# Kernel optimization log

Measured on AMD Instinct MI355X. Metric: run time of the kernel, lower is better.

The kernel has to match this reference:

```python
import jax, jax.numpy as jnp
import numpy as np

H, W, HID = 7, 7, 512
IN_DIM = 1024

def _grid_edges(h, w):
    e = []
    for r in range(h):
        for c in range(w):
            n = r * w + c
            if c < w - 1:
                e.append((n, n + 1))
            if r < h - 1:
                e.append((n, n + w))
    return np.asarray(e, dtype=np.int32).T  # [2, 84]

_BASE = _grid_edges(H, W)

def setup_inputs() -> dict:
    key = jax.random.key(0)
    ks = jax.random.split(key, 16)
    B = 1024
    s = 0.02
    return {
        "visual_feat": jax.random.normal(ks[0], (B, 512, H, W), jnp.float32),
        "tactile_feat": jax.random.normal(ks[1], (B, 512, H, W), jnp.float32),
        "proj_W": jax.random.normal(ks[2], (IN_DIM, 2), jnp.float32) * s,
        "proj_b": jnp.zeros((2,), jnp.float32),
        "gc1_rel_W": jax.random.normal(ks[3], (IN_DIM, HID), jnp.float32) * s,
        "gc1_rel_b": jnp.zeros((HID,), jnp.float32),
        "gc1_root_W": jax.random.normal(ks[4], (IN_DIM, HID), jnp.float32) * s,
        "bn1_gamma": jnp.ones((HID,), jnp.float32),
        "bn1_beta": jnp.zeros((HID,), jnp.float32),
        "gc2_rel_W": jax.random.normal(ks[5], (HID, HID), jnp.float32) * s,
        "gc2_rel_b": jnp.zeros((HID,), jnp.float32),
        "gc2_root_W": jax.random.normal(ks[6], (HID, HID), jnp.float32) * s,
        "bn2_gamma": jnp.ones((HID,), jnp.float32),
        "bn2_beta": jnp.zeros((HID,), jnp.float32),
        "dec_W": jax.random.normal(ks[7], (HID + 1, HID), jnp.float32) * s,
        "dec_b": jnp.zeros((HID,), jnp.float32),
    }

def _batched_edges(B):
    off = (np.arange(B, dtype=np.int32) * (H * W))[:, None]
    src = (_BASE[0][None, :] + off).reshape(-1)
    dst = (_BASE[1][None, :] + off).reshape(-1)
    return jnp.asarray(src), jnp.asarray(dst)

def _bn(x, gamma, beta):
    mu = x.mean(0)
    var = x.var(0)  # biased, matches torch BN normalization
    return (x - mu) * jax.lax.rsqrt(var + 1e-5) * gamma + beta

def _graph_conv(x, src, dst, ew, W_rel, b_rel, W_root, N):
    msg = ew[:, None] * x[src]                      # [E, D]
    agg = jax.ops.segment_sum(msg, dst, num_segments=N)
    deg = jax.ops.segment_sum(jnp.ones_like(ew), dst, num_segments=N)
    agg = agg / jnp.maximum(deg, 1.0)[:, None]
    return agg @ W_rel + b_rel + x @ W_root

def reference(visual_feat, tactile_feat, proj_W, proj_b,
              gc1_rel_W, gc1_rel_b, gc1_root_W, bn1_gamma, bn1_beta,
              gc2_rel_W, gc2_rel_b, gc2_root_W, bn2_gamma, bn2_beta,
              dec_W, dec_b):
    B = visual_feat.shape[0]
    N = B * H * W
    # node features: concat channels, NCHW -> N x (2C)
    node = jnp.concatenate([visual_feat, tactile_feat], axis=1)
    node = node.transpose(0, 2, 3, 1).reshape(N, IN_DIM)
    src, dst = _batched_edges(B)
    coords = node @ proj_W + proj_b                 # [N, 2]
    dist = jnp.linalg.norm(coords[src] - coords[dst], axis=1)
    edge_attr = jax.nn.sigmoid(1.0 / (dist + 1e-6))  # [E]
    alpha = jnp.exp(edge_attr)
    alpha = alpha / (alpha.sum() + 1e-8)            # global normalization over all edges
    x = jax.nn.relu(_bn(_graph_conv(node, src, dst, alpha, gc1_rel_W, gc1_rel_b, gc1_root_W, N), bn1_gamma, bn1_beta))
    x = jax.nn.relu(_bn(_graph_conv(x, src, dst, alpha, gc2_rel_W, gc2_rel_b, gc2_root_W, N), bn2_gamma, bn2_beta))
    # scatter_mean of edge_attr over both endpoints
    ids = jnp.concatenate([src, dst])
    vals = jnp.concatenate([edge_attr, edge_attr])
    nw_sum = jax.ops.segment_sum(vals, ids, num_segments=N)
    nw_cnt = jax.ops.segment_sum(jnp.ones_like(vals), ids, num_segments=N)
    node_w = nw_sum / jnp.maximum(nw_cnt, 1.0)      # [N]
    x = jax.nn.relu(jnp.concatenate([x, node_w[:, None]], axis=1) @ dec_W + dec_b)
    return x.reshape(B, H, W, HID).transpose(0, 3, 1, 2)
```

## Files before the change

kernel.cpp:

```cpp
#include <hip/hip_runtime.h>
#include <hip/hip_bf16.h>

typedef float f32x4 __attribute__((ext_vector_type(4)));
typedef short s16x8 __attribute__((ext_vector_type(8)));

#define N_NODES 50176

static __device__ __forceinline__ ushort f2bf(float x) {
    __hip_bfloat16 h = __float2bfloat16(x);
    return *reinterpret_cast<ushort*>(&h);
}
static __device__ __forceinline__ float bf2f(ushort u) {
    __hip_bfloat16 h = *reinterpret_cast<__hip_bfloat16*>(&u);
    return __bfloat162float(h);
}

static __device__ __forceinline__ void gload_lds16(const void* g, void* l) {
    __builtin_amdgcn_global_load_lds((const __attribute__((address_space(1))) void*)g,
                                     (__attribute__((address_space(3))) void*)l, 16, 0, 0);
}

__global__ void k_prep(const float* W1r, const float* W1t, const float* W2r, const float* W2t,
                       const float* decW, ushort* Bt1, ushort* Bt2, ushort* Bt3, float* decLast,
                       float* alpha_sum, float* bn_acc) {
    int idx = blockIdx.x * 256 + threadIdx.x;
    if (idx < 512 * 2048) {
        int j = idx >> 11, k = idx & 2047;
        float v = (k < 1024) ? W1r[k * 512 + j] : W1t[(k - 1024) * 512 + j];
        Bt1[idx] = f2bf(v);
    }
    if (idx < 512 * 1024) {
        int j = idx >> 10, k = idx & 1023;
        float v = (k < 512) ? W2r[k * 512 + j] : W2t[(k - 512) * 512 + j];
        Bt2[idx] = f2bf(v);
    }
    if (idx < 512 * 512) {
        int j = idx >> 9, k = idx & 511;
        Bt3[idx] = f2bf(decW[k * 512 + j]);
    }
    if (idx < 512) decLast[idx] = decW[512 * 512 + idx];
    if (idx < 2048) bn_acc[idx] = 0.f;
    if (idx == 0) alpha_sum[0] = 0.f;
}

__global__ void k_transpose(const float* vis, const float* tac, ushort* xcat1) {
    int b = blockIdx.x, tid = threadIdx.x;
    __shared__ ushort tile[128 * 50];
    for (int chunk = 0; chunk < 8; ++chunk) {
        const float* src = (chunk < 4 ? vis : tac) + ((size_t)b * 512 + (chunk & 3) * 128) * 49;
        for (int p = tid; p < 128 * 49; p += 256) {
            int d = p / 49, n = p - d * 49;
            tile[d * 50 + n] = f2bf(src[p]);
        }
        __syncthreads();
        for (int p = tid; p < 49 * 64; p += 256) {
            int n = p >> 6, d2 = (p & 63) * 2;
            ushort2 o;
            o.x = tile[d2 * 50 + n];
            o.y = tile[(d2 + 1) * 50 + n];
            *(ushort2*)&xcat1[((size_t)(b * 49 + n)) * 2048 + 1024 + chunk * 128 + d2] = o;
        }
        __syncthreads();
    }
}

__global__ void k_coords(const ushort* xcat1, const float* projW, const float* projb, float* coords) {
    __shared__ float pw[2048];
    int tid = threadIdx.x;
    for (int p = tid; p < 2048; p += 256) pw[p] = projW[p];
    __syncthreads();
    int lane = tid & 63, wave = tid >> 6;
    int n = blockIdx.x * 4 + wave;
    const ushort* row = xcat1 + (size_t)n * 2048 + 1024;
    float c0 = 0.f, c1 = 0.f;
    for (int j = 0; j < 16; ++j) {
        int d = j * 64 + lane;
        float v = bf2f(row[d]);
        c0 += v * pw[2 * d];
        c1 += v * pw[2 * d + 1];
    }
    for (int off = 32; off; off >>= 1) { c0 += __shfl_down(c0, off); c1 += __shfl_down(c1, off); }
    if (lane == 0) { coords[2 * n] = c0 + projb[0]; coords[2 * n + 1] = c1 + projb[1]; }
}

__global__ void k_edges(const float* coords, float* ew_exp, float* node_w, float* alpha_sum) {
    int b = blockIdx.x, tid = threadIdx.x;
    __shared__ float cx[49], cy[49], ea[84];
    __shared__ float wsum[2];
    if (tid < 49) { cx[tid] = coords[(b * 49 + tid) * 2]; cy[tid] = coords[(b * 49 + tid) * 2 + 1]; }
    __syncthreads();
    float ex = 0.f;
    if (tid < 84) {
        int s, d2;
        if (tid < 42) { int r = tid / 6, c = tid - r * 6; s = r * 7 + c; d2 = s + 1; }
        else { int t = tid - 42; int r = t / 7, c = t - r * 7; s = r * 7 + c; d2 = s + 7; }
        float dx = cx[s] - cx[d2], dy = cy[s] - cy[d2];
        float dist = sqrtf(dx * dx + dy * dy);
        float attr = 1.f / (1.f + expf(-(1.f / (dist + 1e-6f))));
        ea[tid] = attr;
        ex = expf(attr);
        ew_exp[b * 84 + tid] = ex;
    }
    for (int off = 32; off; off >>= 1) ex += __shfl_down(ex, off);
    if ((tid & 63) == 0) wsum[tid >> 6] = ex;
    __syncthreads();
    if (tid == 0) atomicAdd(alpha_sum, wsum[0] + wsum[1]);
    if (tid < 49) {
        int r = tid / 7, c = tid - r * 7;
        float s = 0.f; int cnt = 0;
        if (c > 0) { s += ea[r * 6 + c - 1]; cnt++; }
        if (c < 6) { s += ea[r * 6 + c]; cnt++; }
        if (r > 0) { s += ea[42 + (r - 1) * 7 + c]; cnt++; }
        if (r < 6) { s += ea[42 + r * 7 + c]; cnt++; }
        node_w[b * 49 + tid] = s / (float)cnt;
    }
}

__global__ void k_aggin(ushort* __restrict__ xcat, const float* __restrict__ ew,
                        const float* __restrict__ asum) {
    int T = blockIdx.x * 256 + threadIdx.x;
    int n = T >> 7, ch = T & 127;
    int b = n / 49, sp = n - b * 49;
    int r = sp / 7, c = sp - r * 7;
    float acc[8];
#pragma unroll
    for (int k = 0; k < 8; ++k) acc[k] = 0.f;
    int deg = (c > 0) + (r > 0);
    if (deg) {
        float sc = (1.f / (asum[0] + 1e-8f)) / (float)deg;
        if (c > 0) {
            float wl = ew[b * 84 + r * 6 + (c - 1)] * sc;
            s16x8 lv = *(const s16x8*)(xcat + (size_t)(n - 1) * 2048 + 1024 + ch * 8);
#pragma unroll
            for (int k = 0; k < 8; ++k) acc[k] += wl * bf2f((ushort)lv[k]);
        }
        if (r > 0) {
            float wt = ew[b * 84 + 42 + (r - 1) * 7 + c] * sc;
            s16x8 tv = *(const s16x8*)(xcat + (size_t)(n - 7) * 2048 + 1024 + ch * 8);
#pragma unroll
            for (int k = 0; k < 8; ++k) acc[k] += wt * bf2f((ushort)tv[k]);
        }
    }
    s16x8 o;
#pragma unroll
    for (int k = 0; k < 8; ++k) o[k] = (short)f2bf(acc[k]);
    *(s16x8*)(xcat + (size_t)n * 2048 + ch * 8) = o;
}

template <int EPI>
__global__ __launch_bounds__(256, 2)
void k_gemm(const ushort* __restrict__ A, const ushort* __restrict__ Bt, float* __restrict__ C,
            int K,
            const float* __restrict__ bias, float* __restrict__ bn_sum, float* __restrict__ bn_sumsq,
            const float* __restrict__ node_w, const float* __restrict__ decLast,
            const float* __restrict__ decb, float* __restrict__ out) {
    __shared__ __align__(16) ushort As[128 * 32];
    __shared__ __align__(16) ushort Bs[128 * 32];
    const int rowb = blockIdx.x >> 2, colb = blockIdx.x & 3;
    const int row0 = rowb << 7, col0 = colb << 7;
    const int tid = threadIdx.x;
    const int lane = tid & 63, wave = tid >> 6;
    const int wm = (wave & 1) << 6, wn = (wave >> 1) << 6;
    const int quad = lane >> 4, l16 = lane & 15;
    const int K8 = K >> 3;

    const uint4* Ag = (const uint4*)A;
    const uint4* Bg = (const uint4*)Bt;

    const int c0 = wave, c1 = wave + 4;
    const int lrow = lane >> 2, lkc = lane & 3;
    const size_t iA0 = (size_t)(row0 + c0 * 16 + lrow) * K8 + lkc;
    const size_t iA1 = (size_t)(row0 + c1 * 16 + lrow) * K8 + lkc;
    const size_t iB0 = (size_t)(col0 + c0 * 16 + lrow) * K8 + lkc;
    const size_t iB1 = (size_t)(col0 + c1 * 16 + lrow) * K8 + lkc;
    ushort* lA0 = As + c0 * 512;
    ushort* lA1 = As + c1 * 512;
    ushort* lB0 = Bs + c0 * 512;
    ushort* lB1 = Bs + c1 * 512;

    f32x4 acc[4][4];
#pragma unroll
    for (int i = 0; i < 4; ++i)
#pragma unroll
        for (int j = 0; j < 4; ++j) acc[i][j] = (f32x4)0.f;

    const int nk = K >> 5;
    for (int kt = 0; kt < nk; ++kt) {
        const size_t o = (size_t)kt * 4;
        gload_lds16(Ag + iA0 + o, lA0);
        gload_lds16(Ag + iA1 + o, lA1);
        gload_lds16(Bg + iB0 + o, lB0);
        gload_lds16(Bg + iB1 + o, lB1);
        __syncthreads();
        s16x8 af[4], bf[4];
#pragma unroll
        for (int i = 0; i < 4; ++i) af[i] = *(const s16x8*)&As[(wm + i * 16 + l16) * 32 + quad * 8];
#pragma unroll
        for (int j = 0; j < 4; ++j) bf[j] = *(const s16x8*)&Bs[(wn + j * 16 + l16) * 32 + quad * 8];
#pragma unroll
        for (int i = 0; i < 4; ++i)
#pragma unroll
            for (int j = 0; j < 4; ++j)
                acc[i][j] = __builtin_amdgcn_mfma_f32_16x16x32_bf16(af[i], bf[j], acc[i][j], 0, 0, 0);
        __syncthreads();
    }

    if (EPI == 0) {
#pragma unroll
        for (int j = 0; j < 4; ++j) {
            int col = col0 + wn + j * 16 + l16;
            float bcol = bias[col];
            float s = 0.f, s2 = 0.f;
#pragma unroll
            for (int i = 0; i < 4; ++i) {
#pragma unroll
                for (int r = 0; r < 4; ++r) {
                    int m = row0 + wm + i * 16 + quad * 4 + r;
                    float v = acc[i][j][r] + bcol;
                    C[(size_t)m * 512 + col] = v;
                    s += v; s2 += v * v;
                }
            }
            s += __shfl_xor(s, 16); s += __shfl_xor(s, 32);
            s2 += __shfl_xor(s2, 16); s2 += __shfl_xor(s2, 32);
            if (quad == 0) { atomicAdd(&bn_sum[col], s); atomicAdd(&bn_sumsq[col], s2); }
        }
    } else {
#pragma unroll
        for (int i = 0; i < 4; ++i) {
#pragma unroll
            for (int j = 0; j < 4; ++j) {
#pragma unroll
                for (int r = 0; r < 4; ++r) {
                    int m = row0 + wm + i * 16 + quad * 4 + r;
                    int n = col0 + wn + j * 16 + l16;
                    float v = acc[i][j][r];
                    v += node_w[m] * decLast[n] + decb[n];
                    v = fmaxf(v, 0.f);
                    int bb = m / 49, sp = m - bb * 49;
                    out[((size_t)bb * 512 + n) * 49 + sp] = v;
                }
            }
        }
    }
}

__global__ void k_bnstat(const float* bn_sum, const float* bn_sumsq, const float* gamma, const float* beta,
                         float* scale, float* shift) {
    int d = threadIdx.x;
    const float invN = 1.f / (float)N_NODES;
    float mu = bn_sum[d] * invN;
    float var = bn_sumsq[d] * invN - mu * mu;
    float sc = gamma[d] * rsqrtf(var + 1e-5f);
    scale[d] = sc;
    shift[d] = beta[d] - mu * sc;
}

__global__ __launch_bounds__(256) void k_bnagg(const float* __restrict__ P, const float* __restrict__ ew,
                                               const float* __restrict__ asum,
                                               const float* __restrict__ scale, const float* __restrict__ shift,
                                               ushort* __restrict__ xcat) {
    int b = blockIdx.x, tid = threadIdx.x;
    __shared__ ushort xl[49 * 512];
    __shared__ float wl[49], wt[49];
    if (tid < 49) {
        int r = tid / 7, c = tid - r * 7;
        int deg = (c > 0) + (r > 0);
        float sc = deg ? (1.f / (asum[0] + 1e-8f)) / (float)deg : 0.f;
        wl[tid] = (c > 0) ? ew[b * 84 + r * 6 + (c - 1)] * sc : 0.f;
        wt[tid] = (r > 0) ? ew[b * 84 + 42 + (r - 1) * 7 + c] * sc : 0.f;
    }
    int dc = tid & 127;
    int sp0 = tid >> 7;
    float4 scl = ((const float4*)scale)[dc];
    float4 shf = ((const float4*)shift)[dc];
    for (int sp = sp0; sp < 49; sp += 2) {
        float4 v = ((const float4*)(P + ((size_t)b * 49 + sp) * 512))[dc];
        ushort4 o;
        o.x = f2bf(fmaxf(v.x * scl.x + shf.x, 0.f));
        o.y = f2bf(fmaxf(v.y * scl.y + shf.y, 0.f));
        o.z = f2bf(fmaxf(v.z * scl.z + shf.z, 0.f));
        o.w = f2bf(fmaxf(v.w * scl.w + shf.w, 0.f));
        *(ushort4*)&xl[sp * 512 + dc * 4] = o;
        ((ushort4*)(xcat + ((size_t)b * 49 + sp) * 1024 + 512))[dc] = o;
    }
    __syncthreads();
    for (int sp = sp0; sp < 49; sp += 2) {
        float a0 = 0.f, a1 = 0.f, a2 = 0.f, a3 = 0.f;
        float w1 = wl[sp], w2 = wt[sp];
        if (w1 != 0.f) {
            ushort4 u = *(const ushort4*)&xl[(sp - 1) * 512 + dc * 4];
            a0 += w1 * bf2f(u.x); a1 += w1 * bf2f(u.y); a2 += w1 * bf2f(u.z); a3 += w1 * bf2f(u.w);
        }
        if (w2 != 0.f) {
            ushort4 u = *(const ushort4*)&xl[(sp - 7) * 512 + dc * 4];
            a0 += w2 * bf2f(u.x); a1 += w2 * bf2f(u.y); a2 += w2 * bf2f(u.z); a3 += w2 * bf2f(u.w);
        }
        ushort4 o;
        o.x = f2bf(a0); o.y = f2bf(a1); o.z = f2bf(a2); o.w = f2bf(a3);
        ((ushort4*)(xcat + ((size_t)b * 49 + sp) * 1024))[dc] = o;
    }
}

__global__ void k_bnapply(const float* __restrict__ x, const float* __restrict__ scale,
                          const float* __restrict__ shift, ushort* __restrict__ xb) {
    int tid = threadIdx.x;
    size_t i = (size_t)blockIdx.x * 256 + tid;
    int dc = tid & 127;
    float4 scl = ((const float4*)scale)[dc];
    float4 shf = ((const float4*)shift)[dc];
    float4 v = ((const float4*)x)[i];
    ushort4 o;
    o.x = f2bf(fmaxf(v.x * scl.x + shf.x, 0.f));
    o.y = f2bf(fmaxf(v.y * scl.y + shf.y, 0.f));
    o.z = f2bf(fmaxf(v.z * scl.z + shf.z, 0.f));
    o.w = f2bf(fmaxf(v.w * scl.w + shf.w, 0.f));
    ((ushort4*)xb)[i] = o;
}

extern "C" void kernel_launch(void* const* d_in, const int* in_sizes, int n_in,
                              void* d_out, int out_size, void* d_ws, size_t ws_size,
                              hipStream_t stream) {
    const float* vis   = (const float*)d_in[0];
    const float* tac   = (const float*)d_in[1];
    const float* projW = (const float*)d_in[2];
    const float* projb = (const float*)d_in[3];
    const float* W1r   = (const float*)d_in[4];
    const float* b1    = (const float*)d_in[5];
    const float* W1t   = (const float*)d_in[6];
    const float* g1    = (const float*)d_in[7];
    const float* be1   = (const float*)d_in[8];
    const float* W2r   = (const float*)d_in[9];
    const float* b2    = (const float*)d_in[10];
    const float* W2t   = (const float*)d_in[11];
    const float* g2    = (const float*)d_in[12];
    const float* be2   = (const float*)d_in[13];
    const float* decW  = (const float*)d_in[14];
    const float* decb  = (const float*)d_in[15];
    float* out = (float*)d_out;

    char* p = (char*)d_ws;
    ushort* X   = (ushort*)p; p += 205520896;
    float*  P   = (float*)p;  p += 102760448;
    float* coords = (float*)p; p += 401408;
    float* ew     = (float*)p; p += 344064;
    float* nw     = (float*)p; p += 200704;
    ushort* Bt1   = (ushort*)p; p += 2097152;
    ushort* Bt2   = (ushort*)p; p += 1048576;
    ushort* Bt3   = (ushort*)p; p += 524288;
    float* decLast = (float*)p; p += 2048;
    float* asum   = (float*)p;  p += 256;
    float* bnacc  = (float*)p;  p += 4 * 512 * 4;
    float* scsh   = (float*)p;  p += 4 * 512 * 4;
    float* bn1s = bnacc, *bn1q = bnacc + 512, *bn2s = bnacc + 1024, *bn2q = bnacc + 1536;
    float* sc1 = scsh, *sh1 = scsh + 512, *sc2 = scsh + 1024, *sh2 = scsh + 1536;

    ushort* xcat1 = X;
    ushort* xcat2 = X;
    ushort* x3b   = X;

    k_prep<<<4096, 256, 0, stream>>>(W1r, W1t, W2r, W2t, decW, Bt1, Bt2, Bt3, decLast, asum, bnacc);
    k_transpose<<<1024, 256, 0, stream>>>(vis, tac, xcat1);
    k_coords<<<12544, 256, 0, stream>>>(xcat1, projW, projb, coords);
    k_edges<<<1024, 128, 0, stream>>>(coords, ew, nw, asum);
    k_aggin<<<25088, 256, 0, stream>>>(xcat1, ew, asum);

    k_gemm<0><<<392 * 4, 256, 0, stream>>>(xcat1, Bt1, P, 2048, b1, bn1s, bn1q, nullptr, nullptr, nullptr, nullptr);
    k_bnstat<<<1, 512, 0, stream>>>(bn1s, bn1q, g1, be1, sc1, sh1);
    k_bnagg<<<1024, 256, 0, stream>>>(P, ew, asum, sc1, sh1, xcat2);

    k_gemm<0><<<392 * 4, 256, 0, stream>>>(xcat2, Bt2, P, 1024, b2, bn2s, bn2q, nullptr, nullptr, nullptr, nullptr);
    k_bnstat<<<1, 512, 0, stream>>>(bn2s, bn2q, g2, be2, sc2, sh2);
    k_bnapply<<<25088, 256, 0, stream>>>(P, sc2, sh2, x3b);

    k_gemm<1><<<392 * 4, 256, 0, stream>>>(x3b, Bt3, nullptr, 512, nullptr, nullptr, nullptr, nw, decLast, decb, out);
}
```

Baseline: 814.6 us.

## Fuse transpose, coordinate projection and edge weights into one kernel; swizzle GEMM blocks

Merges the transpose, coordinate projection and edge computation into a single per-sample kernel. The projection is computed from the bf16 tile already in LDS, so the transposed features are no longer re-read from global memory and two launches plus the coords buffer go away. The GEMM block index is also remapped so groups of 8 row tiles share column tiles, which is meant to improve L2 reuse of A and B. In exchange the front kernel does more serialized work per block and uses more LDS.

```diff
diff --git a/kernel.cpp b/kernel.cpp
--- a/kernel.cpp
+++ b/kernel.cpp
@@ -43,10 +43,19 @@
     if (idx == 0) alpha_sum[0] = 0.f;
 }
 
-__global__ void k_transpose(const float* vis, const float* tac, ushort* xcat1) {
+__global__ __launch_bounds__(256) void k_front(const float* __restrict__ vis, const float* __restrict__ tac,
+                                               const float* __restrict__ projW, const float* __restrict__ projb,
+                                               ushort* __restrict__ xcat1, float* __restrict__ ew_exp,
+                                               float* __restrict__ node_w, float* __restrict__ alpha_sum) {
     int b = blockIdx.x, tid = threadIdx.x;
     __shared__ ushort tile[128 * 50];
+    __shared__ float pw[2048];
+    __shared__ float cx[52], cy[52], ea[84], wsum[4];
+    for (int p = tid; p < 2048; p += 256) pw[p] = projW[p];
+    float a0t = 0.f, a1t = 0.f;
+    const int cn = tid >> 2, dl = tid & 3;
     for (int chunk = 0; chunk < 8; ++chunk) {
+        __syncthreads();
         const float* src = (chunk < 4 ? vis : tac) + ((size_t)b * 512 + (chunk & 3) * 128) * 49;
         for (int p = tid; p < 128 * 49; p += 256) {
             int d = p / 49, n = p - d * 49;
@@ -60,34 +69,20 @@
             o.y = tile[(d2 + 1) * 50 + n];
             *(ushort2*)&xcat1[((size_t)(b * 49 + n)) * 2048 + 1024 + chunk * 128 + d2] = o;
         }
-        __syncthreads();
-    }
-}
-
-__global__ void k_coords(const ushort* xcat1, const float* projW, const float* projb, float* coords) {
-    __shared__ float pw[2048];
-    int tid = threadIdx.x;
-    for (int p = tid; p < 2048; p += 256) pw[p] = projW[p];
-    __syncthreads();
-    int lane = tid & 63, wave = tid >> 6;
-    int n = blockIdx.x * 4 + wave;
-    const ushort* row = xcat1 + (size_t)n * 2048 + 1024;
-    float c0 = 0.f, c1 = 0.f;
-    for (int j = 0; j < 16; ++j) {
-        int d = j * 64 + lane;
-        float v = bf2f(row[d]);
-        c0 += v * pw[2 * d];
-        c1 += v * pw[2 * d + 1];
-    }
-    for (int off = 32; off; off >>= 1) { c0 += __shfl_down(c0, off); c1 += __shfl_down(c1, off); }
-    if (lane == 0) { coords[2 * n] = c0 + projb[0]; coords[2 * n + 1] = c1 + projb[1]; }
-}
-
-__global__ void k_edges(const float* coords, float* ew_exp, float* node_w, float* alpha_sum) {
-    int b = blockIdx.x, tid = threadIdx.x;
-    __shared__ float cx[49], cy[49], ea[84];
-    __shared__ float wsum[2];
-    if (tid < 49) { cx[tid] = coords[(b * 49 + tid) * 2]; cy[tid] = coords[(b * 49 + tid) * 2 + 1]; }
+        if (tid < 196) {
+#pragma unroll 4
+            for (int j = 0; j < 32; ++j) {
+                int d = dl + 4 * j;
+                float v = bf2f(tile[d * 50 + cn]);
+                int gd = chunk * 128 + d;
+                a0t += v * pw[2 * gd];
+                a1t += v * pw[2 * gd + 1];
+            }
+        }
+    }
+    a0t += __shfl_down(a0t, 1); a1t += __shfl_down(a1t, 1);
+    a0t += __shfl_down(a0t, 2); a1t += __shfl_down(a1t, 2);
+    if (tid < 196 && dl == 0) { cx[cn] = a0t + projb[0]; cy[cn] = a1t + projb[1]; }
     __syncthreads();
     float ex = 0.f;
     if (tid < 84) {
@@ -104,7 +99,7 @@
     for (int off = 32; off; off >>= 1) ex += __shfl_down(ex, off);
     if ((tid & 63) == 0) wsum[tid >> 6] = ex;
     __syncthreads();
-    if (tid == 0) atomicAdd(alpha_sum, wsum[0] + wsum[1]);
+    if (tid == 0) atomicAdd(alpha_sum, wsum[0] + wsum[1] + wsum[2] + wsum[3]);
     if (tid < 49) {
         int r = tid / 7, c = tid - r * 7;
         float s = 0.f; int cnt = 0;
@@ -156,7 +151,9 @@
             const float* __restrict__ decb, float* __restrict__ out) {
     __shared__ __align__(16) ushort As[128 * 32];
     __shared__ __align__(16) ushort Bs[128 * 32];
-    const int rowb = blockIdx.x >> 2, colb = blockIdx.x & 3;
+    const int bid = blockIdx.x;
+    const int rowb = ((bid & 7) | ((bid >> 5) << 3));
+    const int colb = (bid >> 3) & 3;
     const int row0 = rowb << 7, col0 = colb << 7;
     const int tid = threadIdx.x;
     const int lane = tid & 63, wave = tid >> 6;
@@ -342,7 +339,6 @@
     char* p = (char*)d_ws;
     ushort* X   = (ushort*)p; p += 205520896;
     float*  P   = (float*)p;  p += 102760448;
-    float* coords = (float*)p; p += 401408;
     float* ew     = (float*)p; p += 344064;
     float* nw     = (float*)p; p += 200704;
     ushort* Bt1   = (ushort*)p; p += 2097152;
@@ -360,9 +356,7 @@
     ushort* x3b   = X;
 
     k_prep<<<4096, 256, 0, stream>>>(W1r, W1t, W2r, W2t, decW, Bt1, Bt2, Bt3, decLast, asum, bnacc);
-    k_transpose<<<1024, 256, 0, stream>>>(vis, tac, xcat1);
-    k_coords<<<12544, 256, 0, stream>>>(xcat1, projW, projb, coords);
-    k_edges<<<1024, 128, 0, stream>>>(coords, ew, nw, asum);
+    k_front<<<1024, 256, 0, stream>>>(vis, tac, projW, projb, xcat1, ew, nw, asum);
     k_aggin<<<25088, 256, 0, stream>>>(xcat1, ew, asum);
 
     k_gemm<0><<<392 * 4, 256, 0, stream>>>(xcat1, Bt1, P, 2048, b1, bn1s, bn1q, nullptr, nullptr, nullptr, nullptr);
```

Measured after the change: 744.1 us. -8.6%, faster.
